# Kernel optimization log

Measured on AMD Instinct MI355X. Metric: run time of the kernel, lower is better.

## Reference

```python
import jax, jax.numpy as jnp
import numpy as np

NUM_EXPERTS = 64
NUM_SELECTED = 2
HASH_BITS = 32


def setup_inputs() -> dict:
    key = jax.random.key(0)
    k1, k2 = jax.random.split(key)
    hidden_states = jax.random.normal(k1, (4, 4096, 2048), dtype=jnp.float32)
    # torch Linear weight [out_features, in_features], init normal(std=0.01), bias zeros
    hash_w = jax.random.normal(k2, (NUM_SELECTED * HASH_BITS, 2048), dtype=jnp.float32) * 0.01
    hash_b = jnp.zeros((NUM_SELECTED * HASH_BITS,), dtype=jnp.float32)
    return {"hidden_states": hidden_states, "hash_w": hash_w, "hash_b": hash_b}


def reference(hidden_states, hash_w, hash_b):
    B, S, H = hidden_states.shape
    T = B * S
    x = hidden_states.reshape(T, H)
    # hash projection: [T, k*32]
    h = x @ hash_w.T + hash_b
    bits = (h > 0).astype(jnp.int32).reshape(T, NUM_SELECTED, HASH_BITS)
    cand = bits.sum(axis=-1) % NUM_EXPERTS  # [T, k] candidate expert per slot

    # Sequential dedup (vectorized over tokens): for each slot i in order, if the
    # candidate collides with an already-chosen expert for that token, advance
    # (e+1) % E until a free expert is found (always exists since k <= E).
    used = jnp.zeros((T, NUM_EXPERTS), dtype=bool)
    offs = jnp.arange(NUM_EXPERTS)
    chosen = []
    for i in range(NUM_SELECTED):
        e = cand[:, i]  # [T]
        pos = (e[:, None] + offs[None, :]) % NUM_EXPERTS  # [T, E] probe sequence
        probed = jnp.take_along_axis(used, pos, axis=1)  # [T, E] used flags along probe
        off = jnp.argmax(~probed, axis=1)  # first free offset (0 if candidate free)
        ne = (e + off) % NUM_EXPERTS
        used = used | jax.nn.one_hot(ne, NUM_EXPERTS, dtype=bool)
        chosen.append(ne)
    expert_indices = jnp.stack(chosen, axis=1).astype(jnp.int32)  # [T, k]
    expert_weights = jnp.full((T, NUM_SELECTED), 1.0 / NUM_SELECTED, dtype=jnp.float32)
    router_logits = jnp.zeros((T, NUM_EXPERTS), dtype=jnp.float32)
    return expert_weights, expert_indices, router_logits
```

## Files before the change

### kernel.cpp

```cpp
#include <hip/hip_runtime.h>


typedef __attribute__((ext_vector_type(8))) short short8;
typedef __attribute__((ext_vector_type(4))) float f32x4;

constexpr int H    = 2048;
constexpr int NJ   = 64;
constexpr int TOKB = 16;

__device__ __forceinline__ unsigned short bf16_rne(float f) {
    unsigned u = __float_as_uint(f);
    u += 0x7fffu + ((u >> 16) & 1u);
    return (unsigned short)(u >> 16);
}
__device__ __forceinline__ void split1(float f, unsigned short& h, unsigned short& l) {
    h = bf16_rne(f);
    const float hf = __uint_as_float((unsigned)h << 16);
    l = bf16_rne(f - hf);
}

__global__ __launch_bounds__(256) void wcvt_kernel(
    const float* __restrict__ w, unsigned short* __restrict__ wh,
    unsigned short* __restrict__ wl) {
    const int i = (blockIdx.x * 256 + threadIdx.x) * 4;
    const float4 v = *(const float4*)(w + i);
    ushort4 h, l;
    split1(v.x, h.x, l.x); split1(v.y, h.y, l.y);
    split1(v.z, h.z, l.z); split1(v.w, h.w, l.w);
    *(ushort4*)(wh + i) = h;
    *(ushort4*)(wl + i) = l;
}

__global__ __launch_bounds__(256, 4) void hash_router_kernel(
    const float* __restrict__ x,
    const float* __restrict__ w,
    const float* __restrict__ b,
    const unsigned short* __restrict__ wh,
    const unsigned short* __restrict__ wl,
    float* __restrict__ out,
    int T)
{
    __shared__ float red[3][64][17];

    const int tid  = threadIdx.x;
    const int lane = tid & 63;
    const int q    = __builtin_amdgcn_readfirstlane(tid >> 6);
    const int l15  = lane & 15;
    const int quad = lane >> 4;
    const int tok0 = blockIdx.x * TOKB;

    f32x4 acc[4] = {{0.f,0.f,0.f,0.f},{0.f,0.f,0.f,0.f},
                    {0.f,0.f,0.f,0.f},{0.f,0.f,0.f,0.f}};

    const float* xbase = x + (size_t)(tok0 + l15) * H + q * 512 + quad * 8;

#pragma unroll 4
    for (int ks = 0; ks < 16; ++ks) {
        const int kb = ks * 32;
        const float4 a0 = *(const float4*)(xbase + kb);
        const float4 a1 = *(const float4*)(xbase + kb + 4);

        short8 ah, al;
        {
            unsigned short h0,l0,h1,l1,h2,l2,h3,l3;
            split1(a0.x,h0,l0); split1(a0.y,h1,l1); split1(a0.z,h2,l2); split1(a0.w,h3,l3);
            ah[0]=(short)h0; ah[1]=(short)h1; ah[2]=(short)h2; ah[3]=(short)h3;
            al[0]=(short)l0; al[1]=(short)l1; al[2]=(short)l2; al[3]=(short)l3;
            split1(a1.x,h0,l0); split1(a1.y,h1,l1); split1(a1.z,h2,l2); split1(a1.w,h3,l3);
            ah[4]=(short)h0; ah[5]=(short)h1; ah[6]=(short)h2; ah[7]=(short)h3;
            al[4]=(short)l0; al[5]=(short)l1; al[6]=(short)l2; al[7]=(short)l3;
        }

#pragma unroll
        for (int nt = 0; nt < 4; ++nt) {
            const size_t wo = (size_t)(nt * 16 + l15) * H + q * 512 + kb + quad * 8;
            const short8 bh = *(const short8*)(wh + wo);
            const short8 bl = *(const short8*)(wl + wo);
            acc[nt] = __builtin_amdgcn_mfma_f32_16x16x32_bf16(ah, bh, acc[nt], 0, 0, 0);
            acc[nt] = __builtin_amdgcn_mfma_f32_16x16x32_bf16(al, bh, acc[nt], 0, 0, 0);
            acc[nt] = __builtin_amdgcn_mfma_f32_16x16x32_bf16(ah, bl, acc[nt], 0, 0, 0);
        }
    }

    if (q) {
#pragma unroll
        for (int nt = 0; nt < 4; ++nt)
#pragma unroll
            for (int r = 0; r < 4; ++r)
                red[q - 1][lane][nt * 4 + r] = acc[nt][r];
    }
    __syncthreads();

    if (q == 0) {
#pragma unroll
        for (int i = 0; i < 3; ++i)
#pragma unroll
            for (int nt = 0; nt < 4; ++nt)
#pragma unroll
                for (int r = 0; r < 4; ++r)
                    acc[nt][r] += red[i][lane][nt * 4 + r];

        bool pos[4][4];
#pragma unroll
        for (int nt = 0; nt < 4; ++nt) {
            const float bias = b[nt * 16 + l15];
#pragma unroll
            for (int r = 0; r < 4; ++r) {
                const float v = acc[nt][r] + bias;
                bool p;
                if (__builtin_expect(fabsf(v) < 5e-5f, 0)) {
                    const int t = tok0 + quad * 4 + r;
                    const int j = nt * 16 + l15;
                    const float* xr = x + (size_t)t * H;
                    const float* wr = w + (size_t)j * H;
                    double sd = (double)bias;
                    for (int k = 0; k < H; ++k)
                        sd += (double)xr[k] * (double)wr[k];
                    p = (sd > 0.0);
                } else {
                    p = (v > 0.0f);
                }
                pos[nt][r] = p;
            }
        }

        unsigned long long m[4][4];
#pragma unroll
        for (int nt = 0; nt < 4; ++nt)
#pragma unroll
            for (int r = 0; r < 4; ++r)
                m[nt][r] = __ballot(pos[nt][r]);

        if (lane < 16) {
            const int qq = lane >> 2, rr = lane & 3;
            const int c0 = __popcll((m[0][rr] >> (qq * 16)) & 0xffffull)
                         + __popcll((m[1][rr] >> (qq * 16)) & 0xffffull);
            const int c1 = __popcll((m[2][rr] >> (qq * 16)) & 0xffffull)
                         + __popcll((m[3][rr] >> (qq * 16)) & 0xffffull);
            const int t  = tok0 + lane;
            const int i1 = c1 + ((c1 == c0) ? 1 : 0);
            float2 wq; wq.x = 0.5f; wq.y = 0.5f;
            *(float2*)(out + 2 * (size_t)t) = wq;
            float2 iq; iq.x = (float)c0; iq.y = (float)i1;
            *(float2*)(out + 2 * (size_t)T + 2 * (size_t)t) = iq;
        }
    }

    float4 z; z.x = 0.f; z.y = 0.f; z.z = 0.f; z.w = 0.f;
    *(float4*)(out + 4 * (size_t)T + (size_t)tok0 * NJ + tid * 4) = z;
}

extern "C" void kernel_launch(void* const* d_in, const int* in_sizes, int n_in,
                              void* d_out, int out_size, void* d_ws, size_t ws_size,
                              hipStream_t stream) {
    const float* x = (const float*)d_in[0];
    const float* w = (const float*)d_in[1];
    const float* b = (const float*)d_in[2];
    float* out = (float*)d_out;
    const int T = in_sizes[0] / H;
    unsigned short* wh = (unsigned short*)d_ws;
    unsigned short* wl = wh + NJ * H;

    wcvt_kernel<<<dim3(NJ * H / 1024), dim3(256), 0, stream>>>(w, wh, wl);
    hash_router_kernel<<<dim3(T / TOKB), dim3(256), 0, stream>>>(
        x, w, b, wh, wl, out, T);
}
```

Baseline: 308.3 us.

## Stage K-sliced bf16 weight split in LDS and reduce partials in separate kernel

The weight conversion now writes hi/lo bf16 halves in a permuted, MFMA-ready layout grouped by K-slice. The main kernel splits K into four 512-wide slices. Each 1024-thread block copies its slice's weights into 128KB of LDS once and reuses them for 256 tokens. Before, every 16-token block streamed the full weight pair from global/L2. A new reduce kernel sums the four partial slices, adds bias, does the sign-bit counting and dedup, and writes the zero logits. This cuts repeated weight traffic at the cost of a 16MB partial-sum round trip, an extra launch, a hardcoded token count, and one large block per CU.

Result: no change. 302.7 us (-1.8%).

```diff
diff --git a/kernel.cpp b/kernel.cpp
--- a/kernel.cpp
+++ b/kernel.cpp
@@ -4,9 +4,15 @@
 typedef __attribute__((ext_vector_type(8))) short short8;
 typedef __attribute__((ext_vector_type(4))) float f32x4;
 
-constexpr int H    = 2048;
-constexpr int NJ   = 64;
-constexpr int TOKB = 16;
+constexpr int H      = 2048;
+constexpr int NJ     = 64;
+constexpr int T_TOT  = 16384;
+constexpr int KSL    = 512;
+constexpr int NSL    = 4;
+constexpr int NG     = KSL / 32;
+constexpr int UNITS_SL = 32 * 64 * 4;
+constexpr size_t WPERM_UNITS = (size_t)NSL * UNITS_SL;
+constexpr size_t PART_OFF    = WPERM_UNITS * 4;
 
 __device__ __forceinline__ unsigned short bf16_rne(float f) {
     unsigned u = __float_as_uint(f);
@@ -20,124 +26,128 @@
 }
 
 __global__ __launch_bounds__(256) void wcvt_kernel(
-    const float* __restrict__ w, unsigned short* __restrict__ wh,
-    unsigned short* __restrict__ wl) {
-    const int i = (blockIdx.x * 256 + threadIdx.x) * 4;
-    const float4 v = *(const float4*)(w + i);
-    ushort4 h, l;
-    split1(v.x, h.x, l.x); split1(v.y, h.y, l.y);
-    split1(v.z, h.z, l.z); split1(v.w, h.w, l.w);
-    *(ushort4*)(wh + i) = h;
-    *(ushort4*)(wl + i) = l;
+    const float* __restrict__ w, unsigned short* __restrict__ wperm) {
+    const int n   = blockIdx.x * 256 + threadIdx.x;
+    const int quad = n & 3;
+    const int g    = (n >> 2) & 15;
+    const int s    = (n >> 6) & 3;
+    const int row  = n >> 8;
+    const float4 a0 = *(const float4*)(w + (size_t)row * H + s * KSL + g * 32 + quad * 4);
+    const float4 a1 = *(const float4*)(w + (size_t)row * H + s * KSL + g * 32 + 16 + quad * 4);
+    ushort4 h0, l0, h1, l1;
+    split1(a0.x, h0.x, l0.x); split1(a0.y, h0.y, l0.y);
+    split1(a0.z, h0.z, l0.z); split1(a0.w, h0.w, l0.w);
+    split1(a1.x, h1.x, l1.x); split1(a1.y, h1.y, l1.y);
+    split1(a1.z, h1.z, l1.z); split1(a1.w, h1.w, l1.w);
+    const size_t uh = ((size_t)s * UNITS_SL + (g * 2 + 0) * 256 + row * 4 + quad) * 8;
+    const size_t ul = ((size_t)s * UNITS_SL + (g * 2 + 1) * 256 + row * 4 + quad) * 8;
+    *(ushort4*)(wperm + uh)     = h0;
+    *(ushort4*)(wperm + uh + 4) = h1;
+    *(ushort4*)(wperm + ul)     = l0;
+    *(ushort4*)(wperm + ul + 4) = l1;
 }
 
-__global__ __launch_bounds__(256, 4) void hash_router_kernel(
+__global__ __launch_bounds__(1024, 4) void hash_main_kernel(
     const float* __restrict__ x,
-    const float* __restrict__ w,
-    const float* __restrict__ b,
-    const unsigned short* __restrict__ wh,
-    const unsigned short* __restrict__ wl,
-    float* __restrict__ out,
-    int T)
+    const unsigned short* __restrict__ wperm,
+    float* __restrict__ partials)
 {
-    __shared__ float red[3][64][17];
+    __shared__ unsigned short lds[UNITS_SL * 8];
 
     const int tid  = threadIdx.x;
+    const int s    = __builtin_amdgcn_readfirstlane(blockIdx.x >> 6);
+    const int bs   = __builtin_amdgcn_readfirstlane(blockIdx.x & 63);
     const int lane = tid & 63;
-    const int q    = __builtin_amdgcn_readfirstlane(tid >> 6);
+    const int wv   = tid >> 6;
     const int l15  = lane & 15;
     const int quad = lane >> 4;
-    const int tok0 = blockIdx.x * TOKB;
+    const int t0   = bs * 256 + wv * 16;
+
+    {
+        const float4* src = (const float4*)wperm + (size_t)s * UNITS_SL;
+        float4* dst = (float4*)lds;
+#pragma unroll
+        for (int it = 0; it < 8; ++it) {
+            const int u = it * 1024 + tid;
+            dst[u] = src[u];
+        }
+    }
+    __syncthreads();
 
     f32x4 acc[4] = {{0.f,0.f,0.f,0.f},{0.f,0.f,0.f,0.f},
                     {0.f,0.f,0.f,0.f},{0.f,0.f,0.f,0.f}};
 
-    const float* xbase = x + (size_t)(tok0 + l15) * H + q * 512 + quad * 8;
+    const float* xb = x + (size_t)(t0 + l15) * H + s * KSL + quad * 4;
 
-#pragma unroll 4
-    for (int ks = 0; ks < 16; ++ks) {
-        const int kb = ks * 32;
-        const float4 a0 = *(const float4*)(xbase + kb);
-        const float4 a1 = *(const float4*)(xbase + kb + 4);
-
+#pragma unroll 2
+    for (int g = 0; g < NG; ++g) {
+        const float4 a0 = *(const float4*)(xb + g * 32);
+        const float4 a1 = *(const float4*)(xb + g * 32 + 16);
         short8 ah, al;
         {
-            unsigned short h0,l0,h1,l1,h2,l2,h3,l3;
-            split1(a0.x,h0,l0); split1(a0.y,h1,l1); split1(a0.z,h2,l2); split1(a0.w,h3,l3);
-            ah[0]=(short)h0; ah[1]=(short)h1; ah[2]=(short)h2; ah[3]=(short)h3;
-            al[0]=(short)l0; al[1]=(short)l1; al[2]=(short)l2; al[3]=(short)l3;
-            split1(a1.x,h0,l0); split1(a1.y,h1,l1); split1(a1.z,h2,l2); split1(a1.w,h3,l3);
-            ah[4]=(short)h0; ah[5]=(short)h1; ah[6]=(short)h2; ah[7]=(short)h3;
-            al[4]=(short)l0; al[5]=(short)l1; al[6]=(short)l2; al[7]=(short)l3;
+            unsigned short h, l;
+            split1(a0.x, h, l); ah[0] = (short)h; al[0] = (short)l;
+            split1(a0.y, h, l); ah[1] = (short)h; al[1] = (short)l;
+            split1(a0.z, h, l); ah[2] = (short)h; al[2] = (short)l;
+            split1(a0.w, h, l); ah[3] = (short)h; al[3] = (short)l;
+            split1(a1.x, h, l); ah[4] = (short)h; al[4] = (short)l;
+            split1(a1.y, h, l); ah[5] = (short)h; al[5] = (short)l;
+            split1(a1.z, h, l); ah[6] = (short)h; al[6] = (short)l;
+            split1(a1.w, h, l); ah[7] = (short)h; al[7] = (short)l;
         }
-
 #pragma unroll
         for (int nt = 0; nt < 4; ++nt) {
-            const size_t wo = (size_t)(nt * 16 + l15) * H + q * 512 + kb + quad * 8;
-            const short8 bh = *(const short8*)(wh + wo);
-            const short8 bl = *(const short8*)(wl + wo);
+            const short8 bh = *(const short8*)(lds + ((g * 2 + 0) * 256 + nt * 64 + l15 * 4 + quad) * 8);
+            const short8 bl = *(const short8*)(lds + ((g * 2 + 1) * 256 + nt * 64 + l15 * 4 + quad) * 8);
             acc[nt] = __builtin_amdgcn_mfma_f32_16x16x32_bf16(ah, bh, acc[nt], 0, 0, 0);
             acc[nt] = __builtin_amdgcn_mfma_f32_16x16x32_bf16(al, bh, acc[nt], 0, 0, 0);
             acc[nt] = __builtin_amdgcn_mfma_f32_16x16x32_bf16(ah, bl, acc[nt], 0, 0, 0);
         }
     }
 
-    if (q) {
+    float* pb = partials + ((size_t)s * T_TOT + t0) * NJ;
 #pragma unroll
-        for (int nt = 0; nt < 4; ++nt)
+    for (int nt = 0; nt < 4; ++nt)
 #pragma unroll
-            for (int r = 0; r < 4; ++r)
-                red[q - 1][lane][nt * 4 + r] = acc[nt][r];
-    }
-    __syncthreads();
+        for (int r = 0; r < 4; ++r)
+            pb[(quad * 4 + r) * NJ + nt * 16 + l15] = acc[nt][r];
+}
 
-    if (q == 0) {
-#pragma unroll
-        for (int i = 0; i < 3; ++i)
-#pragma unroll
-            for (int nt = 0; nt < 4; ++nt)
-#pragma unroll
-                for (int r = 0; r < 4; ++r)
-                    acc[nt][r] += red[i][lane][nt * 4 + r];
+__global__ __launch_bounds__(256) void hash_reduce_kernel(
+    const float* __restrict__ partials,
+    const float* __restrict__ x,
+    const float* __restrict__ w,
+    const float* __restrict__ b,
+    float* __restrict__ out, int T)
+{
+    const int tid  = threadIdx.x;
+    const int lane = tid & 63;
+    const int wv   = tid >> 6;
+    const int wave_id = blockIdx.x * 4 + wv;
+    const float bias = b[lane];
 
-        bool pos[4][4];
-#pragma unroll
-        for (int nt = 0; nt < 4; ++nt) {
-            const float bias = b[nt * 16 + l15];
-#pragma unroll
-            for (int r = 0; r < 4; ++r) {
-                const float v = acc[nt][r] + bias;
-                bool p;
-                if (__builtin_expect(fabsf(v) < 5e-5f, 0)) {
-                    const int t = tok0 + quad * 4 + r;
-                    const int j = nt * 16 + l15;
-                    const float* xr = x + (size_t)t * H;
-                    const float* wr = w + (size_t)j * H;
-                    double sd = (double)bias;
-                    for (int k = 0; k < H; ++k)
-                        sd += (double)xr[k] * (double)wr[k];
-                    p = (sd > 0.0);
-                } else {
-                    p = (v > 0.0f);
-                }
-                pos[nt][r] = p;
-            }
+    for (int i = 0; i < 16; ++i) {
+        const int t = wave_id * 16 + i;
+        float v = bias;
+        v += partials[((size_t)0 * T_TOT + t) * NJ + lane];
+        v += partials[((size_t)1 * T_TOT + t) * NJ + lane];
+        v += partials[((size_t)2 * T_TOT + t) * NJ + lane];
+        v += partials[((size_t)3 * T_TOT + t) * NJ + lane];
+        bool pos;
+        if (__builtin_expect(fabsf(v) < 5e-5f, 0)) {
+            const float* xr = x + (size_t)t * H;
+            const float* wr = w + (size_t)lane * H;
+            double sd = (double)bias;
+            for (int k = 0; k < H; ++k)
+                sd += (double)xr[k] * (double)wr[k];
+            pos = (sd > 0.0);
+        } else {
+            pos = (v > 0.0f);
         }
-
-        unsigned long long m[4][4];
-#pragma unroll
-        for (int nt = 0; nt < 4; ++nt)
-#pragma unroll
-            for (int r = 0; r < 4; ++r)
-                m[nt][r] = __ballot(pos[nt][r]);
-
-        if (lane < 16) {
-            const int qq = lane >> 2, rr = lane & 3;
-            const int c0 = __popcll((m[0][rr] >> (qq * 16)) & 0xffffull)
-                         + __popcll((m[1][rr] >> (qq * 16)) & 0xffffull);
-            const int c1 = __popcll((m[2][rr] >> (qq * 16)) & 0xffffull)
-                         + __popcll((m[3][rr] >> (qq * 16)) & 0xffffull);
-            const int t  = tok0 + lane;
+        const unsigned long long m = __ballot(pos);
+        if (lane == 0) {
+            const int c0 = __popcll(m & 0xffffffffull);
+            const int c1 = __popcll(m >> 32);
             const int i1 = c1 + ((c1 == c0) ? 1 : 0);
             float2 wq; wq.x = 0.5f; wq.y = 0.5f;
             *(float2*)(out + 2 * (size_t)t) = wq;
@@ -147,7 +157,10 @@
     }
 
     float4 z; z.x = 0.f; z.y = 0.f; z.z = 0.f; z.w = 0.f;
-    *(float4*)(out + 4 * (size_t)T + (size_t)tok0 * NJ + tid * 4) = z;
+    float* lbase = out + 4 * (size_t)T;
+#pragma unroll
+    for (int it = 0; it < 4; ++it)
+        *(float4*)(lbase + (size_t)(it * 65536 + blockIdx.x * 256 + tid) * 4) = z;
 }
 
 extern "C" void kernel_launch(void* const* d_in, const int* in_sizes, int n_in,
@@ -158,10 +171,10 @@
     const float* b = (const float*)d_in[2];
     float* out = (float*)d_out;
     const int T = in_sizes[0] / H;
-    unsigned short* wh = (unsigned short*)d_ws;
-    unsigned short* wl = wh + NJ * H;
+    unsigned short* wperm = (unsigned short*)d_ws;
+    float* partials = (float*)d_ws + PART_OFF;
 
-    wcvt_kernel<<<dim3(NJ * H / 1024), dim3(256), 0, stream>>>(w, wh, wl);
-    hash_router_kernel<<<dim3(T / TOKB), dim3(256), 0, stream>>>(
-        x, w, b, wh, wl, out, T);
+    wcvt_kernel<<<dim3(64), dim3(256), 0, stream>>>(w, wperm);
+    hash_main_kernel<<<dim3(256), dim3(1024), 0, stream>>>(x, wperm, partials);
+    hash_reduce_kernel<<<dim3(256), dim3(256), 0, stream>>>(partials, x, w, b, out, T);
 }
```
